# Performance work log

Measured on AMD Instinct MI355X. Metric: run time of the kernel, lower is better.

The kernel has to match this reference:

```python
import jax, jax.numpy as jnp
import numpy as np

D_MODEL = 1024
N_HEAD = 16
D_HEAD = D_MODEL // N_HEAD
EXP = 4
B, T = 2, 2048
EPS = 1e-5

def setup_inputs() -> dict:
    key = jax.random.key(0)
    ks = jax.random.split(key, 16)
    s = 0.02
    return {
        "x": jax.random.normal(ks[0], (B, T, D_MODEL), jnp.float32),
        "ln1_w": jnp.ones((D_MODEL,), jnp.float32),
        "ln1_b": jnp.zeros((D_MODEL,), jnp.float32),
        "attn_w": jax.random.normal(ks[1], (D_MODEL, 3 * D_MODEL), jnp.float32) * s,
        "attn_b": jnp.zeros((3 * D_MODEL,), jnp.float32),
        "proj_w": jax.random.normal(ks[2], (D_MODEL, D_MODEL), jnp.float32) * s,
        "proj_b": jnp.zeros((D_MODEL,), jnp.float32),
        "ln2_w": jnp.ones((D_MODEL,), jnp.float32),
        "ln2_b": jnp.zeros((D_MODEL,), jnp.float32),
        "fc_w": jax.random.normal(ks[3], (D_MODEL, EXP * D_MODEL), jnp.float32) * s,
        "fc_b": jnp.zeros((EXP * D_MODEL,), jnp.float32),
        "fc2_w": jax.random.normal(ks[4], (EXP * D_MODEL, D_MODEL), jnp.float32) * s,
        "fc2_b": jnp.zeros((D_MODEL,), jnp.float32),
    }

def _layernorm(x, w, b):
    mu = jnp.mean(x, axis=-1, keepdims=True)
    var = jnp.mean(jnp.square(x - mu), axis=-1, keepdims=True)
    return (x - mu) * jax.lax.rsqrt(var + EPS) * w + b

def _attn(x, attn_w, attn_b, proj_w, proj_b):
    Bx, Tx, C = x.shape
    qkv = x @ attn_w + attn_b  # [B,T,3C]
    q, k, v = jnp.split(qkv, 3, axis=-1)
    # [B, H, T, Dh]
    q = q.reshape(Bx, Tx, N_HEAD, D_HEAD).transpose(0, 2, 1, 3)
    k = k.reshape(Bx, Tx, N_HEAD, D_HEAD).transpose(0, 2, 1, 3)
    v = v.reshape(Bx, Tx, N_HEAD, D_HEAD).transpose(0, 2, 1, 3)
    att = jnp.einsum('bhqd,bhkd->bhqk', q, k) * (1.0 / np.sqrt(D_HEAD))
    causal = jnp.tril(jnp.ones((Tx, Tx), bool))
    att = jnp.where(causal, att, -jnp.inf)
    att = jax.nn.softmax(att, axis=-1)
    y = jnp.einsum('bhqk,bhkd->bhqd', att, v)
    y = y.transpose(0, 2, 1, 3).reshape(Bx, Tx, C)
    return y @ proj_w + proj_b

def reference(x, ln1_w, ln1_b, attn_w, attn_b, proj_w, proj_b,
              ln2_w, ln2_b, fc_w, fc_b, fc2_w, fc2_b):
    x = x + _attn(_layernorm(x, ln1_w, ln1_b), attn_w, attn_b, proj_w, proj_b)
    h = _layernorm(x, ln2_w, ln2_b)
    h = jax.nn.gelu(h @ fc_w + fc_b, approximate=False)  # exact GELU (torch nn.GELU default)
    x = x + (h @ fc2_w + fc2_b)
    return x
```

## Files before the change

kernel.cpp:

```cpp
#include <hip/hip_runtime.h>
#include <hip/hip_bf16.h>
#include <math.h>


#define D_MODEL 1024
#define N_HEAD  16
#define D_HEAD  64
#define SEQ_T   2048
#define BATCH   2
#define NROWS   (BATCH * SEQ_T)
#define C3      (3 * D_MODEL)
#define D_FF    (4 * D_MODEL)

typedef __bf16 bf16x8 __attribute__((ext_vector_type(8)));
typedef __bf16 bf16x4t __attribute__((ext_vector_type(4)));
typedef short  s16x4  __attribute__((ext_vector_type(4)));
typedef float  f32x4  __attribute__((ext_vector_type(4)));

#define WAIT_VM8() asm volatile("s_waitcnt vmcnt(8)" ::: "memory")
#define WAIT_VM4() asm volatile("s_waitcnt vmcnt(4)" ::: "memory")

__device__ __forceinline__ f32x4 mfma16_bf16(s16x4 a, s16x4 b, f32x4 c)
{
#if __has_builtin(__builtin_amdgcn_mfma_f32_16x16x16_bf16)
    return __builtin_amdgcn_mfma_f32_16x16x16_bf16(
        __builtin_bit_cast(bf16x4t, a), __builtin_bit_cast(bf16x4t, b), c, 0, 0, 0);
#else
    return __builtin_amdgcn_mfma_f32_16x16x16bf16_1k(a, b, c, 0, 0, 0);
#endif
}

__global__ __launch_bounds__(256) void ln_kernel(
    const float* __restrict__ in, const float* __restrict__ w,
    const float* __restrict__ b, __hip_bfloat16* __restrict__ out, int D)
{
    const int row = blockIdx.x;
    const int tid = threadIdx.x;
    const float* x = in + (size_t)row * D;

    float s = 0.f, s2 = 0.f;
    for (int i = tid; i < D; i += 256) {
        float v = x[i];
        s += v; s2 += v * v;
    }
    __shared__ float rs[256], rs2[256];
    rs[tid] = s; rs2[tid] = s2;
    __syncthreads();
    for (int off = 128; off > 0; off >>= 1) {
        if (tid < off) { rs[tid] += rs[tid + off]; rs2[tid] += rs2[tid + off]; }
        __syncthreads();
    }
    const float mu   = rs[0] / D;
    const float var  = rs2[0] / D - mu * mu;
    const float rstd = rsqrtf(var + 1e-5f);

    __hip_bfloat16* o = out + (size_t)row * D;
    for (int i = tid; i < D; i += 256)
        o[i] = __float2bfloat16((x[i] - mu) * rstd * w[i] + b[i]);
}

__global__ __launch_bounds__(256) void transpose_all_kernel(
    const float* __restrict__ attn_w, const float* __restrict__ proj_w,
    const float* __restrict__ fc_w,   const float* __restrict__ fc2_w,
    __hip_bfloat16* __restrict__ attn_wt, __hip_bfloat16* __restrict__ proj_wt,
    __hip_bfloat16* __restrict__ fc_wt,   __hip_bfloat16* __restrict__ fc2_wt)
{
    __shared__ float t[32][33];
    int tb = blockIdx.x;
    const float* W; __hip_bfloat16* Wt; int K, N;
    if (tb < 3072)      { W = attn_w; Wt = attn_wt; K = D_MODEL; N = C3; }
    else if (tb < 4096) { tb -= 3072; W = proj_w; Wt = proj_wt; K = D_MODEL; N = D_MODEL; }
    else if (tb < 8192) { tb -= 4096; W = fc_w;   Wt = fc_wt;   K = D_MODEL; N = D_FF; }
    else                { tb -= 8192; W = fc2_w;  Wt = fc2_wt;  K = D_FF;    N = D_MODEL; }
    const int ntx = N >> 5;
    const int k0 = (tb / ntx) * 32;
    const int n0 = (tb % ntx) * 32;

    const int tx = threadIdx.x & 31;
    const int ty = threadIdx.x >> 5;
#pragma unroll
    for (int i = 0; i < 4; ++i)
        t[ty + 8 * i][tx] = W[(size_t)(k0 + ty + 8 * i) * N + n0 + tx];
    __syncthreads();
#pragma unroll
    for (int i = 0; i < 4; ++i)
        Wt[(size_t)(n0 + ty + 8 * i) * K + k0 + tx] =
            __float2bfloat16(t[tx][ty + 8 * i]);
}

__device__ __forceinline__ void async16(const __hip_bfloat16* g, __hip_bfloat16* l)
{
    __builtin_amdgcn_global_load_lds(
        (const __attribute__((address_space(1))) void*)g,
        (__attribute__((address_space(3))) void*)l, 16, 0, 0);
}

__device__ __forceinline__ float gelu_exact(float v)
{
    return 0.5f * v * (1.0f + erff(v * 0.70710678118654752f));
}

__device__ __forceinline__ void swz_xcd(int& bx, int& by)
{
    const int nbx = gridDim.x;
    const int nwg = nbx * gridDim.y;
    int lin = blockIdx.y * nbx + blockIdx.x;
    const int per = nwg >> 3;
    lin = (lin & 7) * per + (lin >> 3);
    bx = lin % nbx;
    by = lin / nbx;
}


template<int NL, int TPB>
__device__ __forceinline__ void stage_slice(
    const __hip_bfloat16* __restrict__ g, int K,
    __hip_bfloat16* __restrict__ ldst, int tid)
{
#pragma unroll
    for (int i = 0; i < NL; ++i)
        async16(g + (size_t)(i * (TPB / 4)) * K, ldst + i * (TPB / 4) * 32 + tid * 8);
}

__device__ __forceinline__ void gemm_rot4_512(
    const __hip_bfloat16* __restrict__ A,
    const __hip_bfloat16* __restrict__ Bt,
    int K, int row0, int col0, f32x4 (&acc)[8][4])
{
    __shared__ __align__(16) __hip_bfloat16 Asl[4][256 * 32];
    __shared__ __align__(16) __hip_bfloat16 Bsl[4][256 * 32];

    const int tid  = threadIdx.x;
    const int wv   = tid >> 6;
    const int lane = tid & 63;
    const int ln15 = lane & 15;
    const int lq   = lane >> 4;
    const int mbase = (wv >> 2) * 128;
    const int nbase = (wv & 3) * 64;
    const int rcol = (lq ^ ((ln15 >> 1) & 3)) * 8;
    const int ssw  = ((tid & 3) ^ ((tid >> 3) & 3)) * 8;
    const __hip_bfloat16* Ab = A  + (size_t)(row0 + (tid >> 2)) * K + ssw;
    const __hip_bfloat16* Bb = Bt + (size_t)(col0 + (tid >> 2)) * K + ssw;
    const int nt = K >> 5;

#pragma unroll
    for (int mi = 0; mi < 8; ++mi)
#pragma unroll
        for (int ni = 0; ni < 4; ++ni) acc[mi][ni] = (f32x4){0.f, 0.f, 0.f, 0.f};

#pragma unroll
    for (int t = 0; t < 3; ++t) {
        stage_slice<2, 512>(Ab + t * 32, K, &Asl[t][0], tid);
        stage_slice<2, 512>(Bb + t * 32, K, &Bsl[t][0], tid);
    }
    WAIT_VM8();
    __builtin_amdgcn_s_barrier();

    for (int tq = 0; tq < nt; tq += 4) {
#pragma unroll
        for (int u = 0; u < 4; ++u) {
            const int t   = tq + u;
            const int tcl = (t + 3 < nt) ? t + 3 : nt - 1;
            const int sl  = u;
            const int sl3 = (u + 3) & 3;
            bf16x8 af[4], bfr[4];

#pragma unroll
            for (int mi = 0; mi < 4; ++mi)
                af[mi] = *(const bf16x8*)&Asl[sl][(mbase + mi * 16 + ln15) * 32 + rcol];
#pragma unroll
            for (int ni = 0; ni < 4; ++ni)
                bfr[ni] = *(const bf16x8*)&Bsl[sl][(nbase + ni * 16 + ln15) * 32 + rcol];
            stage_slice<2, 512>(Ab + (size_t)tcl * 32, K, &Asl[sl3][0], tid);
            __builtin_amdgcn_s_barrier();
            __builtin_amdgcn_s_setprio(1);
#pragma unroll
            for (int mi = 0; mi < 4; ++mi)
#pragma unroll
                for (int ni = 0; ni < 4; ++ni)
                    acc[mi][ni] = __builtin_amdgcn_mfma_f32_16x16x32_bf16(
                        af[mi], bfr[ni], acc[mi][ni], 0, 0, 0);
            __builtin_amdgcn_s_setprio(0);
            __builtin_amdgcn_s_barrier();

#pragma unroll
            for (int mi = 0; mi < 4; ++mi)
                af[mi] = *(const bf16x8*)&Asl[sl][(mbase + 64 + mi * 16 + ln15) * 32 + rcol];
            stage_slice<2, 512>(Bb + (size_t)tcl * 32, K, &Bsl[sl3][0], tid);
            WAIT_VM8();
            __builtin_amdgcn_s_barrier();
            __builtin_amdgcn_s_setprio(1);
#pragma unroll
            for (int mi = 0; mi < 4; ++mi)
#pragma unroll
                for (int ni = 0; ni < 4; ++ni)
                    acc[4 + mi][ni] = __builtin_amdgcn_mfma_f32_16x16x32_bf16(
                        af[mi], bfr[ni], acc[4 + mi][ni], 0, 0, 0);
            __builtin_amdgcn_s_setprio(0);
            __builtin_amdgcn_s_barrier();
        }
    }
}

__device__ __forceinline__ void gemm_rot4_128x8(
    const __hip_bfloat16* __restrict__ A,
    const __hip_bfloat16* __restrict__ Bt,
    int K, int row0, int col0, f32x4 (&acc)[2][4])
{
    __shared__ __align__(16) __hip_bfloat16 Asl[4][128 * 32];
    __shared__ __align__(16) __hip_bfloat16 Bsl[4][128 * 32];

    const int tid  = threadIdx.x;
    const int wv   = tid >> 6;
    const int lane = tid & 63;
    const int ln15 = lane & 15;
    const int lq   = lane >> 4;
    const int mbase = (wv >> 1) * 32;
    const int nbase = (wv & 1) * 64;
    const int rcol = (lq ^ ((ln15 >> 1) & 3)) * 8;
    const int ssw  = ((tid & 3) ^ ((tid >> 3) & 3)) * 8;
    const __hip_bfloat16* Ab = A  + (size_t)(row0 + (tid >> 2)) * K + ssw;
    const __hip_bfloat16* Bb = Bt + (size_t)(col0 + (tid >> 2)) * K + ssw;
    const int nt = K >> 5;

#pragma unroll
    for (int mi = 0; mi < 2; ++mi)
#pragma unroll
        for (int ni = 0; ni < 4; ++ni) acc[mi][ni] = (f32x4){0.f, 0.f, 0.f, 0.f};

#pragma unroll
    for (int t = 0; t < 3; ++t) {
        stage_slice<1, 512>(Ab + t * 32, K, &Asl[t][0], tid);
        stage_slice<1, 512>(Bb + t * 32, K, &Bsl[t][0], tid);
    }
    WAIT_VM4();
    __builtin_amdgcn_s_barrier();

    for (int tq = 0; tq < nt; tq += 4) {
#pragma unroll
        for (int u = 0; u < 4; ++u) {
            const int t   = tq + u;
            const int tcl = (t + 3 < nt) ? t + 3 : nt - 1;
            const int sl  = u;
            const int sl3 = (u + 3) & 3;
            bf16x8 af[2], bfr[4];

#pragma unroll
            for (int mi = 0; mi < 2; ++mi)
                af[mi] = *(const bf16x8*)&Asl[sl][(mbase + mi * 16 + ln15) * 32 + rcol];
#pragma unroll
            for (int ni = 0; ni < 4; ++ni)
                bfr[ni] = *(const bf16x8*)&Bsl[sl][(nbase + ni * 16 + ln15) * 32 + rcol];
            stage_slice<1, 512>(Ab + (size_t)tcl * 32, K, &Asl[sl3][0], tid);
            stage_slice<1, 512>(Bb + (size_t)tcl * 32, K, &Bsl[sl3][0], tid);
            WAIT_VM4();
            __builtin_amdgcn_s_barrier();
            __builtin_amdgcn_s_setprio(1);
#pragma unroll
            for (int mi = 0; mi < 2; ++mi)
#pragma unroll
                for (int ni = 0; ni < 4; ++ni)
                    acc[mi][ni] = __builtin_amdgcn_mfma_f32_16x16x32_bf16(
                        af[mi], bfr[ni], acc[mi][ni], 0, 0, 0);
            __builtin_amdgcn_s_setprio(0);
            __builtin_amdgcn_s_barrier();
        }
    }
}

__global__ __launch_bounds__(512) void gemm256_kernel(
    const __hip_bfloat16* __restrict__ A,
    const __hip_bfloat16* __restrict__ Bt,
    const float* __restrict__ bias,
    const float* __restrict__ residual,
    void* __restrict__ Cout,
    int M, int N, int K, int act, int outBf16)
{
    int bx, by;
    swz_xcd(bx, by);
    const int row0 = by * 256;
    const int col0 = bx * 256;

    f32x4 acc[8][4];
    gemm_rot4_512(A, Bt, K, row0, col0, acc);

    const int tid  = threadIdx.x;
    const int wv   = tid >> 6;
    const int lane = tid & 63;
    const int ln15 = lane & 15;
    const int lq   = lane >> 4;
    const int mbase = (wv >> 2) * 128;
    const int nbase = (wv & 3) * 64;

#pragma unroll
    for (int mi = 0; mi < 8; ++mi) {
#pragma unroll
        for (int ni = 0; ni < 4; ++ni) {
            const int gc = col0 + nbase + ni * 16 + ln15;
            const float bv = bias[gc];
#pragma unroll
            for (int r = 0; r < 4; ++r) {
                const int gr = row0 + mbase + mi * 16 + lq * 4 + r;
                float v = acc[mi][ni][r] + bv;
                if (act == 1) v = gelu_exact(v);
                if (residual) v += residual[(size_t)gr * N + gc];
                if (outBf16)
                    ((__hip_bfloat16*)Cout)[(size_t)gr * N + gc] = __float2bfloat16(v);
                else
                    ((float*)Cout)[(size_t)gr * N + gc] = v;
            }
        }
    }
}

__global__ __launch_bounds__(512, 2) void gemm128_kernel(
    const __hip_bfloat16* __restrict__ A,
    const __hip_bfloat16* __restrict__ Bt,
    const float* __restrict__ bias,
    const float* __restrict__ residual,
    void* __restrict__ Cout,
    int M, int N, int K, int act, int outBf16)
{
    int bx, by;
    swz_xcd(bx, by);
    const int row0 = by * 128;
    const int col0 = bx * 128;

    f32x4 acc[2][4];
    gemm_rot4_128x8(A, Bt, K, row0, col0, acc);

    const int tid  = threadIdx.x;
    const int wv   = tid >> 6;
    const int lane = tid & 63;
    const int ln15 = lane & 15;
    const int lq   = lane >> 4;
    const int mbase = (wv >> 1) * 32;
    const int nbase = (wv & 1) * 64;

#pragma unroll
    for (int mi = 0; mi < 2; ++mi) {
#pragma unroll
        for (int ni = 0; ni < 4; ++ni) {
            const int gc = col0 + nbase + ni * 16 + ln15;
            const float bv = bias[gc];
#pragma unroll
            for (int r = 0; r < 4; ++r) {
                const int gr = row0 + mbase + mi * 16 + lq * 4 + r;
                float v = acc[mi][ni][r] + bv;
                if (act == 1) v = gelu_exact(v);
                if (residual) v += residual[(size_t)gr * N + gc];
                if (outBf16)
                    ((__hip_bfloat16*)Cout)[(size_t)gr * N + gc] = __float2bfloat16(v);
                else
                    ((float*)Cout)[(size_t)gr * N + gc] = v;
            }
        }
    }
}

__global__ __launch_bounds__(512) void qkv256_kernel(
    const __hip_bfloat16* __restrict__ A,
    const __hip_bfloat16* __restrict__ Bt,
    const float* __restrict__ bias,
    __hip_bfloat16* __restrict__ Qb,
    __hip_bfloat16* __restrict__ Kb,
    __hip_bfloat16* __restrict__ Vtb)
{
    int bx, by;
    swz_xcd(bx, by);
    const int row0 = by * 256;
    const int col0 = bx * 256;

    f32x4 acc[8][4];
    gemm_rot4_512(A, Bt, D_MODEL, row0, col0, acc);

    const int tid  = threadIdx.x;
    const int wv   = tid >> 6;
    const int lane = tid & 63;
    const int ln15 = lane & 15;
    const int lq   = lane >> 4;
    const int mbase = (wv >> 2) * 128;
    const int nbase = (wv & 3) * 64;

#pragma unroll
    for (int mi = 0; mi < 8; ++mi) {
        const int gr0 = row0 + mbase + mi * 16 + lq * 4;
        const int bb  = gr0 >> 11;
        const int q0  = gr0 & 2047;
#pragma unroll
        for (int ni = 0; ni < 4; ++ni) {
            const int gc  = col0 + nbase + ni * 16 + ln15;
            const float bv = bias[gc];
            const int sec = gc >> 10;
            const int hd  = (gc & 1023) >> 6;
            const int d   = gc & 63;
            if (sec == 2) {
                unsigned short u[4];
#pragma unroll
                for (int r = 0; r < 4; ++r) {
                    __hip_bfloat16 e = __float2bfloat16(acc[mi][ni][r] + bv);
                    u[r] = *(unsigned short*)&e;
                }
                uint2 pk;
                pk.x = (unsigned int)u[0] | ((unsigned int)u[1] << 16);
                pk.y = (unsigned int)u[2] | ((unsigned int)u[3] << 16);
                *(uint2*)(Vtb + ((size_t)((bb * N_HEAD + hd) * D_HEAD + d)) * SEQ_T + q0) = pk;
            } else {
                __hip_bfloat16* dst = (sec == 0 ? Qb : Kb)
                    + ((size_t)((bb * N_HEAD + hd) * SEQ_T + q0)) * D_HEAD + d;
#pragma unroll
                for (int r = 0; r < 4; ++r)
                    dst[(size_t)r * D_HEAD] = __float2bfloat16(acc[mi][ni][r] + bv);
            }
        }
    }
}

#define ATQ 64
#define ATK 128
#define NQT (SEQ_T / ATQ)
#define VP2 136

__global__ __launch_bounds__(256) void mfma_attn_kernel(
    const __hip_bfloat16* __restrict__ Qb,
    const __hip_bfloat16* __restrict__ Kb,
    const __hip_bfloat16* __restrict__ Vtb,
    __hip_bfloat16* __restrict__ y)
{
    __shared__ __align__(16) __hip_bfloat16 Ks[2 * ATK * 32];
    __shared__ __align__(16) __hip_bfloat16 Vts[D_HEAD * VP2];

    const int flat = (blockIdx.z * gridDim.y + blockIdx.y) * gridDim.x + blockIdx.x;
    const int xcd  = flat & 7;
    const int slot = flat >> 3;
    const int pair = slot & 15;
    const int hb   = slot >> 4;
    const int h    = xcd + 8 * (hb & 1);
    const int b    = hb >> 1;

    const int tid  = threadIdx.x;
    const int wv   = tid >> 6;
    const int lane = tid & 63;
    const int ln15 = lane & 15;
    const int lq   = lane >> 4;

    const __hip_bfloat16* Qh = Qb  + (size_t)(b * N_HEAD + h) * SEQ_T * D_HEAD;
    const __hip_bfloat16* Kh = Kb  + (size_t)(b * N_HEAD + h) * SEQ_T * D_HEAD;
    const __hip_bfloat16* Vh = Vtb + (size_t)(b * N_HEAD + h) * D_HEAD * SEQ_T;
    const size_t bT = (size_t)b * SEQ_T;

    const float CEXP = 0.18033688011f;

    bf16x8 kreg[4], vreg[4];
    const int kr = tid >> 3, kg = tid & 7;
    const int vr = tid >> 4, vc = tid & 15;
    const int khalf = kg >> 2;
    const int kpos  = (kg & 3) ^ ((kr >> 1) & 3);

    auto issue = [&](int kb) {
#pragma unroll
        for (int i = 0; i < 4; ++i)
            kreg[i] = *(const bf16x8*)(Kh + (size_t)(kb + kr + i * 32) * D_HEAD + kg * 8);
#pragma unroll
        for (int i = 0; i < 4; ++i)
            vreg[i] = *(const bf16x8*)(Vh + (size_t)(vr + i * 16) * SEQ_T + kb + vc * 8);
    };
    auto commit = [&]() {
#pragma unroll
        for (int i = 0; i < 4; ++i) {
            const int r = kr + i * 32;
            *(bf16x8*)&Ks[khalf * (ATK * 32) + r * 32 + kpos * 8] = kreg[i];
        }
#pragma unroll
        for (int i = 0; i < 4; ++i) {
            const int r = vr + i * 16;
            *(bf16x8*)&Vts[r * VP2 + vc * 8] = vreg[i];
        }
    };

    const int rcol = (lq ^ ((ln15 >> 1) & 3)) * 8;

#pragma unroll 1
    for (int half = 0; half < 2; ++half) {
        const int qt    = half == 0 ? pair : (NQT - 1 - pair);
        const int qbase = qt * ATQ;
        const int ntk   = (qt >> 1) + 1;
        const int qg    = qbase + wv * 16 + ln15;

        bf16x8 qf[2];
#pragma unroll
        for (int kc = 0; kc < 2; ++kc)
            qf[kc] = *(const bf16x8*)(Qh + (size_t)(qbase + wv * 16 + ln15) * D_HEAD
                                      + kc * 32 + lq * 8);

        f32x4 Oacc[4];
#pragma unroll
        for (int dn = 0; dn < 4; ++dn) Oacc[dn] = (f32x4){0.f, 0.f, 0.f, 0.f};
        float m_run = -INFINITY, l_run = 0.f;

        issue(0);

        for (int t = 0; t < ntk; ++t) {
            const int kb = t * ATK;
            commit();
            __syncthreads();
            if (t + 1 < ntk) issue((t + 1) * ATK);

            f32x4 st[8];
#pragma unroll
            for (int jf = 0; jf < 8; ++jf) st[jf] = (f32x4){0.f, 0.f, 0.f, 0.f};
            __builtin_amdgcn_s_setprio(1);
#pragma unroll
            for (int jf = 0; jf < 8; ++jf) {
                const int rw = jf * 16 + ln15;
                const bf16x8 kf0 = *(const bf16x8*)&Ks[rw * 32 + rcol];
                const bf16x8 kf1 = *(const bf16x8*)&Ks[ATK * 32 + rw * 32 + rcol];
                st[jf] = __builtin_amdgcn_mfma_f32_16x16x32_bf16(kf0, qf[0], st[jf], 0, 0, 0);
                st[jf] = __builtin_amdgcn_mfma_f32_16x16x32_bf16(kf1, qf[1], st[jf], 0, 0, 0);
            }
            __builtin_amdgcn_s_setprio(0);

            if (t == ntk - 1) {
#pragma unroll
                for (int jf = 0; jf < 8; ++jf)
#pragma unroll
                    for (int r = 0; r < 4; ++r)
                        if ((kb + jf * 16 + lq * 4 + r) > qg) st[jf][r] = -INFINITY;
            }

            float tmax = st[0][0];
#pragma unroll
            for (int jf = 0; jf < 8; ++jf)
#pragma unroll
                for (int r = 0; r < 4; ++r) tmax = fmaxf(tmax, st[jf][r]);
            tmax = fmaxf(tmax, __shfl_xor(tmax, 16));
            tmax = fmaxf(tmax, __shfl_xor(tmax, 32));
            const float mnew  = fmaxf(m_run, tmax);
            const float alpha = exp2f((m_run - mnew) * CEXP);
            const float mc    = mnew * CEXP;
            float psum = 0.f;
#pragma unroll
            for (int jf = 0; jf < 8; ++jf)
#pragma unroll
                for (int r = 0; r < 4; ++r) {
                    const float p = exp2f(fmaf(st[jf][r], CEXP, -mc));
                    st[jf][r] = p;
                    psum += p;
                }
            psum += __shfl_xor(psum, 16);
            psum += __shfl_xor(psum, 32);
            l_run = alpha * l_run + psum;
            m_run = mnew;

            float a4[4];
#pragma unroll
            for (int r = 0; r < 4; ++r) a4[r] = __shfl(alpha, lq * 4 + r);
#pragma unroll
            for (int dn = 0; dn < 4; ++dn)
#pragma unroll
                for (int r = 0; r < 4; ++r) Oacc[dn][r] *= a4[r];

            __builtin_amdgcn_s_setprio(1);
#pragma unroll
            for (int jf = 0; jf < 8; ++jf) {
                s16x4 pfr;
#pragma unroll
                for (int s = 0; s < 4; ++s) {
                    __hip_bfloat16 e = __float2bfloat16(st[jf][s]);
                    pfr[s] = __builtin_bit_cast(short, e);
                }
#pragma unroll
                for (int dn = 0; dn < 4; ++dn) {
                    const s16x4 vfr = *(const s16x4*)&Vts[(dn * 16 + ln15) * VP2
                                                          + jf * 16 + lq * 4];
                    Oacc[dn] = mfma16_bf16(pfr, vfr, Oacc[dn]);
                }
            }
            __builtin_amdgcn_s_setprio(0);
            __syncthreads();
        }

        float il[4];
#pragma unroll
        for (int r = 0; r < 4; ++r) il[r] = 1.0f / __shfl(l_run, lq * 4 + r);
#pragma unroll
        for (int dn = 0; dn < 4; ++dn)
#pragma unroll
            for (int r = 0; r < 4; ++r)
                Ks[(wv * 16 + lq * 4 + r) * 72 + dn * 16 + ln15] =
                    __float2bfloat16(Oacc[dn][r] * il[r]);
        const int r2 = lane >> 3, c8 = (lane & 7) * 8;
#pragma unroll
        for (int i = 0; i < 2; ++i) {
            const int row = wv * 16 + r2 + 8 * i;
            const bf16x8 val = *(const bf16x8*)&Ks[row * 72 + c8];
            *(bf16x8*)(y + (bT + qbase + row) * D_MODEL + h * D_HEAD + c8) = val;
        }
        __syncthreads();
    }
}

extern "C" void kernel_launch(void* const* d_in, const int* in_sizes, int n_in,
                              void* d_out, int out_size, void* d_ws, size_t ws_size,
                              hipStream_t stream)
{
    const float* x      = (const float*)d_in[0];
    const float* ln1_w  = (const float*)d_in[1];
    const float* ln1_b  = (const float*)d_in[2];
    const float* attn_w = (const float*)d_in[3];
    const float* attn_b = (const float*)d_in[4];
    const float* proj_w = (const float*)d_in[5];
    const float* proj_b = (const float*)d_in[6];
    const float* ln2_w  = (const float*)d_in[7];
    const float* ln2_b  = (const float*)d_in[8];
    const float* fc_w   = (const float*)d_in[9];
    const float* fc_b   = (const float*)d_in[10];
    const float* fc2_w  = (const float*)d_in[11];
    const float* fc2_b  = (const float*)d_in[12];
    float* out = (float*)d_out;

    char* ws = (char*)d_ws;
    __hip_bfloat16* Qb      = (__hip_bfloat16*)(ws);
    __hip_bfloat16* Kb      = (__hip_bfloat16*)(ws + (size_t)8  * 1024 * 1024);
    __hip_bfloat16* Vtb     = (__hip_bfloat16*)(ws + (size_t)16 * 1024 * 1024);
    __hip_bfloat16* h_bf    = (__hip_bfloat16*)(ws);
    __hip_bfloat16* ln_buf  = (__hip_bfloat16*)(ws + (size_t)32 * 1024 * 1024);
    __hip_bfloat16* y_buf   = (__hip_bfloat16*)(ws + (size_t)40 * 1024 * 1024);
    float*          xmid    = (float*)(ws + (size_t)48 * 1024 * 1024);
    __hip_bfloat16* attn_wt = (__hip_bfloat16*)(ws + (size_t)64 * 1024 * 1024);
    __hip_bfloat16* proj_wt = (__hip_bfloat16*)(ws + (size_t)70 * 1024 * 1024);
    __hip_bfloat16* fc_wt   = (__hip_bfloat16*)(ws + (size_t)72 * 1024 * 1024);
    __hip_bfloat16* fc2_wt  = (__hip_bfloat16*)(ws + (size_t)80 * 1024 * 1024);

    dim3 blk256(256);
    dim3 blk512(512);

    transpose_all_kernel<<<dim3(12288), blk256, 0, stream>>>(
        attn_w, proj_w, fc_w, fc2_w, attn_wt, proj_wt, fc_wt, fc2_wt);

    ln_kernel<<<dim3(NROWS), blk256, 0, stream>>>(x, ln1_w, ln1_b, ln_buf, D_MODEL);

    qkv256_kernel<<<dim3(C3 / 256, NROWS / 256), blk512, 0, stream>>>(
        ln_buf, attn_wt, attn_b, Qb, Kb, Vtb);

    mfma_attn_kernel<<<dim3(NQT / 2, N_HEAD, BATCH), blk256, 0, stream>>>(
        Qb, Kb, Vtb, y_buf);

    gemm128_kernel<<<dim3(D_MODEL / 128, NROWS / 128), blk512, 0, stream>>>(
        y_buf, proj_wt, proj_b, x, xmid, NROWS, D_MODEL, D_MODEL, 0, 0);

    ln_kernel<<<dim3(NROWS), blk256, 0, stream>>>(xmid, ln2_w, ln2_b, ln_buf, D_MODEL);

    gemm256_kernel<<<dim3(D_FF / 256, NROWS / 256), blk512, 0, stream>>>(
        ln_buf, fc_wt, fc_b, nullptr, h_bf, NROWS, D_FF, D_MODEL, 1, 1);

    gemm128_kernel<<<dim3(D_MODEL / 128, NROWS / 128), blk512, 0, stream>>>(
        h_bf, fc2_wt, fc2_b, xmid, out, NROWS, D_MODEL, D_FF, 0, 0);
}
```

Measured before the change: 360.2 us.

## Replace 4-stage 256/512-thread GEMM pipelines with double-buffered 128-tile GEMM; vectorize LN/transpose

Swaps the 256x256 (512-thread, 4-slot rotating LDS pipeline) and 128x128 (512-thread) GEMM cores for a single 128x128, 256-thread, double-buffered GEMM used for QKV, proj, FC and FC2, with launch bounds targeting 3 blocks per CU. LayerNorm and the weight transpose are also vectorized to float4 loads and packed bf16 stores. The intent is smaller LDS footprint, more resident blocks and a simpler schedule, but it drops deeper prefetch and waits for all loads (vmcnt 0) every k-step. It also lowers data reuse for the large FC GEMM.

```diff
diff --git a/kernel.cpp b/kernel.cpp
--- a/kernel.cpp
+++ b/kernel.cpp
@@ -17,8 +17,7 @@
 typedef short  s16x4  __attribute__((ext_vector_type(4)));
 typedef float  f32x4  __attribute__((ext_vector_type(4)));
 
-#define WAIT_VM8() asm volatile("s_waitcnt vmcnt(8)" ::: "memory")
-#define WAIT_VM4() asm volatile("s_waitcnt vmcnt(4)" ::: "memory")
+#define WAIT_VM0() asm volatile("s_waitcnt vmcnt(0)" ::: "memory")
 
 __device__ __forceinline__ f32x4 mfma16_bf16(s16x4 a, s16x4 b, f32x4 c)
 {
@@ -36,13 +35,12 @@
 {
     const int row = blockIdx.x;
     const int tid = threadIdx.x;
-    const float* x = in + (size_t)row * D;
-
-    float s = 0.f, s2 = 0.f;
-    for (int i = tid; i < D; i += 256) {
-        float v = x[i];
-        s += v; s2 += v * v;
-    }
+    const float* x = in + (size_t)row * 1024;
+
+    const float4 v = *(const float4*)(x + tid * 4);
+    float s  = v.x + v.y + v.z + v.w;
+    float s2 = v.x * v.x + v.y * v.y + v.z * v.z + v.w * v.w;
+
     __shared__ float rs[256], rs2[256];
     rs[tid] = s; rs2[tid] = s2;
     __syncthreads();
@@ -50,13 +48,22 @@
         if (tid < off) { rs[tid] += rs[tid + off]; rs2[tid] += rs2[tid + off]; }
         __syncthreads();
     }
-    const float mu   = rs[0] / D;
-    const float var  = rs2[0] / D - mu * mu;
+    const float mu   = rs[0] * (1.0f / 1024.0f);
+    const float var  = rs2[0] * (1.0f / 1024.0f) - mu * mu;
     const float rstd = rsqrtf(var + 1e-5f);
 
-    __hip_bfloat16* o = out + (size_t)row * D;
-    for (int i = tid; i < D; i += 256)
-        o[i] = __float2bfloat16((x[i] - mu) * rstd * w[i] + b[i]);
+    const float4 w4 = *(const float4*)(w + tid * 4);
+    const float4 b4 = *(const float4*)(b + tid * 4);
+    float o[4] = {(v.x - mu) * rstd * w4.x + b4.x,
+                  (v.y - mu) * rstd * w4.y + b4.y,
+                  (v.z - mu) * rstd * w4.z + b4.z,
+                  (v.w - mu) * rstd * w4.w + b4.w};
+    ushort4 pk;
+    { __hip_bfloat16 e0 = __float2bfloat16(o[0]); pk.x = *(unsigned short*)&e0;
+      __hip_bfloat16 e1 = __float2bfloat16(o[1]); pk.y = *(unsigned short*)&e1;
+      __hip_bfloat16 e2 = __float2bfloat16(o[2]); pk.z = *(unsigned short*)&e2;
+      __hip_bfloat16 e3 = __float2bfloat16(o[3]); pk.w = *(unsigned short*)&e3; }
+    *(ushort4*)(out + (size_t)row * 1024 + tid * 4) = pk;
 }
 
 __global__ __launch_bounds__(256) void transpose_all_kernel(
@@ -76,16 +83,20 @@
     const int k0 = (tb / ntx) * 32;
     const int n0 = (tb % ntx) * 32;
 
-    const int tx = threadIdx.x & 31;
-    const int ty = threadIdx.x >> 5;
-#pragma unroll
-    for (int i = 0; i < 4; ++i)
-        t[ty + 8 * i][tx] = W[(size_t)(k0 + ty + 8 * i) * N + n0 + tx];
+    const int row = threadIdx.x >> 3;
+    const int c4  = (threadIdx.x & 7) * 4;
+
+    const float4 v = *(const float4*)&W[(size_t)(k0 + row) * N + n0 + c4];
+    t[row][c4 + 0] = v.x; t[row][c4 + 1] = v.y;
+    t[row][c4 + 2] = v.z; t[row][c4 + 3] = v.w;
     __syncthreads();
-#pragma unroll
-    for (int i = 0; i < 4; ++i)
-        Wt[(size_t)(n0 + ty + 8 * i) * K + k0 + tx] =
-            __float2bfloat16(t[tx][ty + 8 * i]);
+
+    ushort4 pk;
+    { __hip_bfloat16 e0 = __float2bfloat16(t[c4 + 0][row]); pk.x = *(unsigned short*)&e0;
+      __hip_bfloat16 e1 = __float2bfloat16(t[c4 + 1][row]); pk.y = *(unsigned short*)&e1;
+      __hip_bfloat16 e2 = __float2bfloat16(t[c4 + 2][row]); pk.z = *(unsigned short*)&e2;
+      __hip_bfloat16 e3 = __float2bfloat16(t[c4 + 3][row]); pk.w = *(unsigned short*)&e3; }
+    *(ushort4*)&Wt[(size_t)(n0 + row) * K + k0 + c4] = pk;
 }
 
 __device__ __forceinline__ void async16(const __hip_bfloat16* g, __hip_bfloat16* l)
@@ -112,110 +123,33 @@
 }
 
 
-template<int NL, int TPB>
-__device__ __forceinline__ void stage_slice(
-    const __hip_bfloat16* __restrict__ g, int K,
-    __hip_bfloat16* __restrict__ ldst, int tid)
-{
-#pragma unroll
-    for (int i = 0; i < NL; ++i)
-        async16(g + (size_t)(i * (TPB / 4)) * K, ldst + i * (TPB / 4) * 32 + tid * 8);
-}
-
-__device__ __forceinline__ void gemm_rot4_512(
+__device__ __forceinline__ void stage_128(
+    const __hip_bfloat16* __restrict__ Ab, const __hip_bfloat16* __restrict__ Bb,
+    int K, int kt, __hip_bfloat16* __restrict__ as,
+    __hip_bfloat16* __restrict__ bs, int tid)
+{
+    const int k0 = kt * 32;
+#pragma unroll
+    for (int i = 0; i < 2; ++i) {
+        async16(Ab + (size_t)(i * 64) * K + k0, as + i * 64 * 32 + tid * 8);
+        async16(Bb + (size_t)(i * 64) * K + k0, bs + i * 64 * 32 + tid * 8);
+    }
+}
+
+__device__ __forceinline__ void gemm_db_256(
     const __hip_bfloat16* __restrict__ A,
     const __hip_bfloat16* __restrict__ Bt,
-    int K, int row0, int col0, f32x4 (&acc)[8][4])
-{
-    __shared__ __align__(16) __hip_bfloat16 Asl[4][256 * 32];
-    __shared__ __align__(16) __hip_bfloat16 Bsl[4][256 * 32];
+    int K, int row0, int col0, f32x4 (&acc)[4][4])
+{
+    __shared__ __align__(16) __hip_bfloat16 Asl[2][128 * 32];
+    __shared__ __align__(16) __hip_bfloat16 Bsl[2][128 * 32];
 
     const int tid  = threadIdx.x;
     const int wv   = tid >> 6;
     const int lane = tid & 63;
     const int ln15 = lane & 15;
     const int lq   = lane >> 4;
-    const int mbase = (wv >> 2) * 128;
-    const int nbase = (wv & 3) * 64;
-    const int rcol = (lq ^ ((ln15 >> 1) & 3)) * 8;
-    const int ssw  = ((tid & 3) ^ ((tid >> 3) & 3)) * 8;
-    const __hip_bfloat16* Ab = A  + (size_t)(row0 + (tid >> 2)) * K + ssw;
-    const __hip_bfloat16* Bb = Bt + (size_t)(col0 + (tid >> 2)) * K + ssw;
-    const int nt = K >> 5;
-
-#pragma unroll
-    for (int mi = 0; mi < 8; ++mi)
-#pragma unroll
-        for (int ni = 0; ni < 4; ++ni) acc[mi][ni] = (f32x4){0.f, 0.f, 0.f, 0.f};
-
-#pragma unroll
-    for (int t = 0; t < 3; ++t) {
-        stage_slice<2, 512>(Ab + t * 32, K, &Asl[t][0], tid);
-        stage_slice<2, 512>(Bb + t * 32, K, &Bsl[t][0], tid);
-    }
-    WAIT_VM8();
-    __builtin_amdgcn_s_barrier();
-
-    for (int tq = 0; tq < nt; tq += 4) {
-#pragma unroll
-        for (int u = 0; u < 4; ++u) {
-            const int t   = tq + u;
-            const int tcl = (t + 3 < nt) ? t + 3 : nt - 1;
-            const int sl  = u;
-            const int sl3 = (u + 3) & 3;
-            bf16x8 af[4], bfr[4];
-
-#pragma unroll
-            for (int mi = 0; mi < 4; ++mi)
-                af[mi] = *(const bf16x8*)&Asl[sl][(mbase + mi * 16 + ln15) * 32 + rcol];
-#pragma unroll
-            for (int ni = 0; ni < 4; ++ni)
-                bfr[ni] = *(const bf16x8*)&Bsl[sl][(nbase + ni * 16 + ln15) * 32 + rcol];
-            stage_slice<2, 512>(Ab + (size_t)tcl * 32, K, &Asl[sl3][0], tid);
-            __builtin_amdgcn_s_barrier();
-            __builtin_amdgcn_s_setprio(1);
-#pragma unroll
-            for (int mi = 0; mi < 4; ++mi)
-#pragma unroll
-                for (int ni = 0; ni < 4; ++ni)
-                    acc[mi][ni] = __builtin_amdgcn_mfma_f32_16x16x32_bf16(
-                        af[mi], bfr[ni], acc[mi][ni], 0, 0, 0);
-            __builtin_amdgcn_s_setprio(0);
-            __builtin_amdgcn_s_barrier();
-
-#pragma unroll
-            for (int mi = 0; mi < 4; ++mi)
-                af[mi] = *(const bf16x8*)&Asl[sl][(mbase + 64 + mi * 16 + ln15) * 32 + rcol];
-            stage_slice<2, 512>(Bb + (size_t)tcl * 32, K, &Bsl[sl3][0], tid);
-            WAIT_VM8();
-            __builtin_amdgcn_s_barrier();
-            __builtin_amdgcn_s_setprio(1);
-#pragma unroll
-            for (int mi = 0; mi < 4; ++mi)
-#pragma unroll
-                for (int ni = 0; ni < 4; ++ni)
-                    acc[4 + mi][ni] = __builtin_amdgcn_mfma_f32_16x16x32_bf16(
-                        af[mi], bfr[ni], acc[4 + mi][ni], 0, 0, 0);
-            __builtin_amdgcn_s_setprio(0);
-            __builtin_amdgcn_s_barrier();
-        }
-    }
-}
-
-__device__ __forceinline__ void gemm_rot4_128x8(
-    const __hip_bfloat16* __restrict__ A,
-    const __hip_bfloat16* __restrict__ Bt,
-    int K, int row0, int col0, f32x4 (&acc)[2][4])
-{
-    __shared__ __align__(16) __hip_bfloat16 Asl[4][128 * 32];
-    __shared__ __align__(16) __hip_bfloat16 Bsl[4][128 * 32];
-
-    const int tid  = threadIdx.x;
-    const int wv   = tid >> 6;
-    const int lane = tid & 63;
-    const int ln15 = lane & 15;
-    const int lq   = lane >> 4;
-    const int mbase = (wv >> 1) * 32;
+    const int mbase = (wv >> 1) * 64;
     const int nbase = (wv & 1) * 64;
     const int rcol = (lq ^ ((ln15 >> 1) & 3)) * 8;
     const int ssw  = ((tid & 3) ^ ((tid >> 3) & 3)) * 8;
@@ -224,51 +158,43 @@
     const int nt = K >> 5;
 
 #pragma unroll
-    for (int mi = 0; mi < 2; ++mi)
+    for (int mi = 0; mi < 4; ++mi)
 #pragma unroll
         for (int ni = 0; ni < 4; ++ni) acc[mi][ni] = (f32x4){0.f, 0.f, 0.f, 0.f};
 
-#pragma unroll
-    for (int t = 0; t < 3; ++t) {
-        stage_slice<1, 512>(Ab + t * 32, K, &Asl[t][0], tid);
-        stage_slice<1, 512>(Bb + t * 32, K, &Bsl[t][0], tid);
+    stage_128(Ab, Bb, K, 0, &Asl[0][0], &Bsl[0][0], tid);
+    WAIT_VM0();
+    __builtin_amdgcn_s_barrier();
+
+    for (int t = 0; t < nt; ++t) {
+        const int p   = t & 1;
+        const int tcl = (t + 1 < nt) ? t + 1 : nt - 1;
+        bf16x8 af[4], bfr[4];
+
+#pragma unroll
+        for (int mi = 0; mi < 4; ++mi)
+            af[mi] = *(const bf16x8*)&Asl[p][(mbase + mi * 16 + ln15) * 32 + rcol];
+#pragma unroll
+        for (int ni = 0; ni < 4; ++ni)
+            bfr[ni] = *(const bf16x8*)&Bsl[p][(nbase + ni * 16 + ln15) * 32 + rcol];
+
+        stage_128(Ab, Bb, K, tcl, &Asl[p ^ 1][0], &Bsl[p ^ 1][0], tid);
+
+        __builtin_amdgcn_s_setprio(1);
+#pragma unroll
+        for (int mi = 0; mi < 4; ++mi)
+#pragma unroll
+            for (int ni = 0; ni < 4; ++ni)
+                acc[mi][ni] = __builtin_amdgcn_mfma_f32_16x16x32_bf16(
+                    af[mi], bfr[ni], acc[mi][ni], 0, 0, 0);
+        __builtin_amdgcn_s_setprio(0);
+
+        WAIT_VM0();
+        __builtin_amdgcn_s_barrier();
     }
-    WAIT_VM4();
-    __builtin_amdgcn_s_barrier();
-
-    for (int tq = 0; tq < nt; tq += 4) {
-#pragma unroll
-        for (int u = 0; u < 4; ++u) {
-            const int t   = tq + u;
-            const int tcl = (t + 3 < nt) ? t + 3 : nt - 1;
-            const int sl  = u;
-            const int sl3 = (u + 3) & 3;
-            bf16x8 af[2], bfr[4];
-
-#pragma unroll
-            for (int mi = 0; mi < 2; ++mi)
-                af[mi] = *(const bf16x8*)&Asl[sl][(mbase + mi * 16 + ln15) * 32 + rcol];
-#pragma unroll
-            for (int ni = 0; ni < 4; ++ni)
-                bfr[ni] = *(const bf16x8*)&Bsl[sl][(nbase + ni * 16 + ln15) * 32 + rcol];
-            stage_slice<1, 512>(Ab + (size_t)tcl * 32, K, &Asl[sl3][0], tid);
-            stage_slice<1, 512>(Bb + (size_t)tcl * 32, K, &Bsl[sl3][0], tid);
-            WAIT_VM4();
-            __builtin_amdgcn_s_barrier();
-            __builtin_amdgcn_s_setprio(1);
-#pragma unroll
-            for (int mi = 0; mi < 2; ++mi)
-#pragma unroll
-                for (int ni = 0; ni < 4; ++ni)
-                    acc[mi][ni] = __builtin_amdgcn_mfma_f32_16x16x32_bf16(
-                        af[mi], bfr[ni], acc[mi][ni], 0, 0, 0);
-            __builtin_amdgcn_s_setprio(0);
-            __builtin_amdgcn_s_barrier();
-        }
-    }
-}
-
-__global__ __launch_bounds__(512) void gemm256_kernel(
+}
+
+__global__ __launch_bounds__(256, 3) void gemm128_kernel(
     const __hip_bfloat16* __restrict__ A,
     const __hip_bfloat16* __restrict__ Bt,
     const float* __restrict__ bias,
@@ -278,22 +204,22 @@
 {
     int bx, by;
     swz_xcd(bx, by);
-    const int row0 = by * 256;
-    const int col0 = bx * 256;
-
-    f32x4 acc[8][4];
-    gemm_rot4_512(A, Bt, K, row0, col0, acc);
+    const int row0 = by * 128;
+    const int col0 = bx * 128;
+
+    f32x4 acc[4][4];
+    gemm_db_256(A, Bt, K, row0, col0, acc);
 
     const int tid  = threadIdx.x;
     const int wv   = tid >> 6;
     const int lane = tid & 63;
     const int ln15 = lane & 15;
     const int lq   = lane >> 4;
-    const int mbase = (wv >> 2) * 128;
-    const int nbase = (wv & 3) * 64;
-
-#pragma unroll
-    for (int mi = 0; mi < 8; ++mi) {
+    const int mbase = (wv >> 1) * 64;
+    const int nbase = (wv & 1) * 64;
+
+#pragma unroll
+    for (int mi = 0; mi < 4; ++mi) {
 #pragma unroll
         for (int ni = 0; ni < 4; ++ni) {
             const int gc = col0 + nbase + ni * 16 + ln15;
@@ -313,52 +239,7 @@
     }
 }
 
-__global__ __launch_bounds__(512, 2) void gemm128_kernel(
-    const __hip_bfloat16* __restrict__ A,
-    const __hip_bfloat16* __restrict__ Bt,
-    const float* __restrict__ bias,
-    const float* __restrict__ residual,
-    void* __restrict__ Cout,
-    int M, int N, int K, int act, int outBf16)
-{
-    int bx, by;
-    swz_xcd(bx, by);
-    const int row0 = by * 128;
-    const int col0 = bx * 128;
-
-    f32x4 acc[2][4];
-    gemm_rot4_128x8(A, Bt, K, row0, col0, acc);
-
-    const int tid  = threadIdx.x;
-    const int wv   = tid >> 6;
-    const int lane = tid & 63;
-    const int ln15 = lane & 15;
-    const int lq   = lane >> 4;
-    const int mbase = (wv >> 1) * 32;
-    const int nbase = (wv & 1) * 64;
-
-#pragma unroll
-    for (int mi = 0; mi < 2; ++mi) {
-#pragma unroll
-        for (int ni = 0; ni < 4; ++ni) {
-            const int gc = col0 + nbase + ni * 16 + ln15;
-            const float bv = bias[gc];
-#pragma unroll
-            for (int r = 0; r < 4; ++r) {
-                const int gr = row0 + mbase + mi * 16 + lq * 4 + r;
-                float v = acc[mi][ni][r] + bv;
-                if (act == 1) v = gelu_exact(v);
-                if (residual) v += residual[(size_t)gr * N + gc];
-                if (outBf16)
-                    ((__hip_bfloat16*)Cout)[(size_t)gr * N + gc] = __float2bfloat16(v);
-                else
-                    ((float*)Cout)[(size_t)gr * N + gc] = v;
-            }
-        }
-    }
-}
-
-__global__ __launch_bounds__(512) void qkv256_kernel(
+__global__ __launch_bounds__(256, 3) void qkv128_kernel(
     const __hip_bfloat16* __restrict__ A,
     const __hip_bfloat16* __restrict__ Bt,
     const float* __restrict__ bias,
@@ -368,22 +249,22 @@
 {
     int bx, by;
     swz_xcd(bx, by);
-    const int row0 = by * 256;
-    const int col0 = bx * 256;
-
-    f32x4 acc[8][4];
-    gemm_rot4_512(A, Bt, D_MODEL, row0, col0, acc);
+    const int row0 = by * 128;
+    const int col0 = bx * 128;
+
+    f32x4 acc[4][4];
+    gemm_db_256(A, Bt, D_MODEL, row0, col0, acc);
 
     const int tid  = threadIdx.x;
     const int wv   = tid >> 6;
     const int lane = tid & 63;
     const int ln15 = lane & 15;
     const int lq   = lane >> 4;
-    const int mbase = (wv >> 2) * 128;
-    const int nbase = (wv & 3) * 64;
-
-#pragma unroll
-    for (int mi = 0; mi < 8; ++mi) {
+    const int mbase = (wv >> 1) * 64;
+    const int nbase = (wv & 1) * 64;
+
+#pragma unroll
+    for (int mi = 0; mi < 4; ++mi) {
         const int gr0 = row0 + mbase + mi * 16 + lq * 4;
         const int bb  = gr0 >> 11;
         const int q0  = gr0 & 2047;
@@ -633,27 +514,26 @@
     __hip_bfloat16* fc2_wt  = (__hip_bfloat16*)(ws + (size_t)80 * 1024 * 1024);
 
     dim3 blk256(256);
-    dim3 blk512(512);
 
     transpose_all_kernel<<<dim3(12288), blk256, 0, stream>>>(
         attn_w, proj_w, fc_w, fc2_w, attn_wt, proj_wt, fc_wt, fc2_wt);
 
     ln_kernel<<<dim3(NROWS), blk256, 0, stream>>>(x, ln1_w, ln1_b, ln_buf, D_MODEL);
 
-    qkv256_kernel<<<dim3(C3 / 256, NROWS / 256), blk512, 0, stream>>>(
+    qkv128_kernel<<<dim3(C3 / 128, NROWS / 128), blk256, 0, stream>>>(
         ln_buf, attn_wt, attn_b, Qb, Kb, Vtb);
 
     mfma_attn_kernel<<<dim3(NQT / 2, N_HEAD, BATCH), blk256, 0, stream>>>(
         Qb, Kb, Vtb, y_buf);
 
-    gemm128_kernel<<<dim3(D_MODEL / 128, NROWS / 128), blk512, 0, stream>>>(
+    gemm128_kernel<<<dim3(D_MODEL / 128, NROWS / 128), blk256, 0, stream>>>(
         y_buf, proj_wt, proj_b, x, xmid, NROWS, D_MODEL, D_MODEL, 0, 0);
 
     ln_kernel<<<dim3(NROWS), blk256, 0, stream>>>(xmid, ln2_w, ln2_b, ln_buf, D_MODEL);
 
-    gemm256_kernel<<<dim3(D_FF / 256, NROWS / 256), blk512, 0, stream>>>(
+    gemm128_kernel<<<dim3(D_FF / 128, NROWS / 128), blk256, 0, stream>>>(
         ln_buf, fc_wt, fc_b, nullptr, h_bf, NROWS, D_FF, D_MODEL, 1, 1);
 
-    gemm128_kernel<<<dim3(D_MODEL / 128, NROWS / 128), blk512, 0, stream>>>(
+    gemm128_kernel<<<dim3(D_MODEL / 128, NROWS / 128), blk256, 0, stream>>>(
         h_bf, fc2_wt, fc2_b, xmid, out, NROWS, D_MODEL, D_FF, 0, 0);
 }
```

Measured after the change: 378.5 us. +5.1%, slower.
